# Kernel tuning notes

Measured on AMD Instinct MI355X. Metric: run time of the kernel, lower is better.

The kernel has to match this reference:

```python
import jax, jax.numpy as jnp
import numpy as np

B, S, E, H, WIN = 1, 2048, 1024, 16, 256
D = E // H  # head_out = 64


def setup_inputs() -> dict:
    key = jax.random.key(0)
    ks = jax.random.split(key, 10)
    w = lambda k: jax.random.normal(k, (E, E), jnp.float32) * 0.02
    return {
        'x': jax.random.normal(ks[0], (B, S, E), jnp.float32),
        'global_attention_mask': jax.random.randint(ks[1], (B, S), 0, 2).astype(jnp.int32),
        'W_local_query': w(ks[2]),
        'W_local_key': w(ks[3]),
        'W_local_value': w(ks[4]),
        'W_query': w(ks[5]),
        'W_key': w(ks[6]),
        'W_value': w(ks[7]),
        'W_proj': w(ks[8]),
        'b_proj': jnp.zeros((E,), jnp.float32),
    }


def reference(x, global_attention_mask, W_local_query, W_local_key, W_local_value,
              W_query, W_key, W_value, W_proj, b_proj):
    b, seq, emb = x.shape
    nH, dh, win = H, D, WIN
    chunks = seq // win
    NEG = -1e9
    scale = 1.0 / (dh ** 0.5)

    # ---- local (windowed) branch ----
    ql = x @ W_local_query            # [b,S,E]
    kl = x @ W_local_key
    vl = x @ W_local_value
    # NOTE: original does a direct .view -> plain reshape (no head transpose)
    qc = ql.reshape(b, nH, chunks, win, dh)
    kc = kl.reshape(b, nH, chunks, win, dh)
    vloc = vl.reshape(b, nH, seq, dh)
    s = jnp.einsum('bhcqd,bhckd->bhcqk', qc, kc)      # [b,H,C,W,W]
    causal_w = jnp.tril(jnp.ones((win, win), bool))
    s = jnp.where(causal_w, s, NEG) * scale           # mask then /sqrt(d), as in source
    s = s.mean(axis=2)                                # mean over chunks -> [b,H,W,W]
    s = jnp.pad(s, ((0, 0), (0, 0), (0, seq - win), (0, seq - win)))
    aw_l = jax.nn.softmax(s, axis=-1)                 # [b,H,S,S]
    local_ctx = jnp.einsum('bhqk,bhkd->bqhd', aw_l, vloc).reshape(b, seq, emb)

    # ---- global (full) branch ----
    q = (x @ W_query).reshape(b, seq, nH, dh).transpose(0, 2, 1, 3)
    k = (x @ W_key).reshape(b, seq, nH, dh).transpose(0, 2, 1, 3)
    v = (x @ W_value).reshape(b, seq, nH, dh).transpose(0, 2, 1, 3)
    sg = jnp.einsum('bhqd,bhkd->bhqk', q, k)          # [b,H,S,S]
    causal_s = jnp.tril(jnp.ones((seq, seq), bool))
    sg = jnp.where(causal_s, sg, NEG) * scale
    aw_g = jax.nn.softmax(sg, axis=-1)
    gctx = jnp.einsum('bhqk,bhkd->bqhd', aw_g, v).reshape(b, seq, emb)

    # ---- combine via global mask, then output projection ----
    ctx = jnp.where(global_attention_mask[:, :, None] == 1, gctx, local_ctx)
    return ctx @ W_proj + b_proj
```

## Files before the change

kernel.cpp:

```cpp
#include <hip/hip_runtime.h>
#include <hip/hip_bf16.h>

typedef _Float16 h8 __attribute__((ext_vector_type(8)));
typedef _Float16 h4 __attribute__((ext_vector_type(4)));
typedef _Float16 h2 __attribute__((ext_vector_type(2)));
typedef __fp16 fp16x2 __attribute__((ext_vector_type(2)));
typedef float f4 __attribute__((ext_vector_type(4)));

#define S_LEN 2048
#define EMB 1024
#define NH 16
#define DH 64

__device__ __forceinline__ void async_copy16(const void* g, void* l) {
  __builtin_amdgcn_global_load_lds(
      (const __attribute__((address_space(1))) void*)g,
      (__attribute__((address_space(3))) void*)l, 16, 0, 0);
}

__device__ __forceinline__ f4 mfma16(h8 a, h8 b, f4 c) {
  return __builtin_amdgcn_mfma_f32_16x16x32_f16(a, b, c, 0, 0, 0);
}

__device__ __forceinline__ h2 cvt_pk(float a, float b) {
  const fp16x2 r = __builtin_amdgcn_cvt_pkrtz(a, b);
  return __builtin_bit_cast(h2, r);
}

__global__ __launch_bounds__(256) void prep_kernel(
    const float* __restrict__ x, const float* w0, const float* w1, const float* w2,
    const float* w3, const float* w4, const float* w5, const float* w6,
    _Float16* __restrict__ xh, _Float16* __restrict__ Wtb) {
  const int bid = blockIdx.x;
  if (bid < 2048) {
    const int i = bid * 256 + threadIdx.x;
    const float4 v = *(const float4*)&x[(long)i * 4];
    h4 o;
    o.x = (_Float16)v.x; o.y = (_Float16)v.y; o.z = (_Float16)v.z; o.w = (_Float16)v.w;
    *(h4*)&xh[(long)i * 4] = o;
    return;
  }
  const int b2 = bid - 2048;
  const int z = b2 >> 10, rem = b2 & 1023;
  const float* W = w0;
  switch (z) {
    case 1: W = w1; break; case 2: W = w2; break; case 3: W = w3; break;
    case 4: W = w4; break; case 5: W = w5; break; case 6: W = w6; break;
    default: break;
  }
  __shared__ float t[32][33];
  const int bk = (rem & 31) * 32, bn = (rem >> 5) * 32;
  const int tx = threadIdx.x & 31, ty = threadIdx.x >> 5;
  #pragma unroll
  for (int i = 0; i < 4; ++i)
    t[ty + i * 8][tx] = W[(long)(bk + ty + i * 8) * 1024 + bn + tx];
  __syncthreads();
  _Float16* o = Wtb + (long)z * 1048576;
  #pragma unroll
  for (int i = 0; i < 4; ++i)
    o[(long)(bn + ty + i * 8) * 1024 + bk + tx] = (_Float16)t[tx][ty + i * 8];
}

__global__ __launch_bounds__(256) void shuffle_kernel(
    const _Float16* __restrict__ ql, const _Float16* __restrict__ kl,
    const _Float16* __restrict__ vl, const _Float16* __restrict__ vg,
    const int* __restrict__ gmask,
    _Float16* __restrict__ Aq, _Float16* __restrict__ Ak,
    _Float16* __restrict__ vgT, float* __restrict__ Vall, float* __restrict__ Vtail,
    int* __restrict__ qsel, int* __restrict__ qcnt) {
  const int bid = blockIdx.x;
  if (bid < 2048) {
    const _Float16* src = (bid >= 1024) ? kl : ql;
    _Float16* dst = (bid >= 1024) ? Ak : Aq;
    const int u = (bid & 1023) * 256 + threadIdx.x;
    const int dseg = u & 7, c = (u >> 3) & 7, q = (u >> 6) & 255, h = u >> 14;
    const long soff = (long)(h * 128 + c * 16 + (q >> 4)) * 1024 + (q & 15) * 64 + dseg * 8;
    *(h8*)&dst[(long)u * 8] = *(const h8*)&src[soff];
    return;
  }
  if (bid < 4096) {
    const int b2 = bid - 2048;
    __shared__ _Float16 t[32][33];
    const int bs = (b2 & 63) * 32, be = (b2 >> 6) * 32;
    const int tx = threadIdx.x & 31, ty = threadIdx.x >> 5;
    #pragma unroll
    for (int i = 0; i < 4; ++i)
      t[ty + i * 8][tx] = vg[(long)(bs + ty + i * 8) * 1024 + be + tx];
    __syncthreads();
    #pragma unroll
    for (int i = 0; i < 4; ++i)
      vgT[(long)(be + ty + i * 8) * 2048 + bs + tx] = t[tx][ty + i * 8];
    return;
  }
  if (bid < 4112) {
    const int hh = bid - 4096;
    const int d = threadIdx.x & 63, g = threadIdx.x >> 6;
    float sall = 0.f, shead = 0.f;
    for (int i = 0; i < 32; ++i) {
      const int ro = g * 32 + i;
      const _Float16* base = vl + (long)(hh * 128 + ro) * 1024 + d;
      #pragma unroll
      for (int j = 0; j < 16; ++j) {
        const float v = (float)base[j * 64];
        sall += v;
        if (ro < 16) shead += v;
      }
    }
    __shared__ float sA[4][64], sH[4][64];
    sA[g][d] = sall; sH[g][d] = shead;
    __syncthreads();
    if (g == 0) {
      const float a = sA[0][d] + sA[1][d] + sA[2][d] + sA[3][d];
      const float hsum = sH[0][d] + sH[1][d] + sH[2][d] + sH[3][d];
      Vall[hh * 64 + d] = a;
      Vtail[hh * 64 + d] = a - hsum;
    }
    return;
  }
  const int t = threadIdx.x;
  int m8[8], cnt8 = 0;
  #pragma unroll
  for (int j = 0; j < 8; ++j) {
    m8[j] = gmask[t * 8 + j];
    cnt8 += (m8[j] == 1);
  }
  __shared__ int sc[256];
  sc[t] = cnt8;
  __syncthreads();
  for (int off = 1; off < 256; off <<= 1) {
    const int v = (t >= off) ? sc[t - off] : 0;
    __syncthreads();
    sc[t] += v;
    __syncthreads();
  }
  int base = sc[t] - cnt8;
  #pragma unroll
  for (int j = 0; j < 8; ++j)
    if (m8[j] == 1) qsel[base++] = t * 8 + j;
  if (t == 255) qcnt[0] = sc[255];
}

__global__ __launch_bounds__(512, 2) void gemm256_kernel(
    const _Float16* __restrict__ A, const _Float16* __restrict__ Bt,
    _Float16* __restrict__ C) {
  const int bid = blockIdx.x;
  const int bxx = (bid >> 3) & 7;
  const int byy = (bid & 7) * 3 + (bid >> 6);
  const int bm = bxx * 256, bn = byy * 256;

  __shared__ alignas(16) _Float16 As[2][2][8192];
  __shared__ alignas(16) _Float16 Bs[2][2][8192];

  const int tid = threadIdx.x;
  const int w = tid >> 6, l = tid & 63;
  const int lo = l & 15, hi = l >> 4;
  const int wm = w >> 2, wn = w & 3;
  const int srow = tid >> 3;
  const int kseg = (tid & 7) ^ (srow & 7);

  const _Float16* Bb = Bt + (long)(byy >> 2) * 1048576 + (long)(bn & 1023) * 1024;

#define STG_A(db, half, tt) do {                                                     \
    const int t_ = (tt) < 15 ? (tt) : 15;                                            \
    const _Float16* s_ = A + (long)(bm + (half) * 128 + srow) * 1024 + t_ * 64 + kseg * 8; \
    async_copy16(s_, &As[db][half][w * 512]);                                        \
    async_copy16(s_ + 65536, &As[db][half][4096 + w * 512]);                         \
  } while (0)
#define STG_B(db, half, tt) do {                                                     \
    const int t_ = (tt) < 15 ? (tt) : 15;                                            \
    const _Float16* s_ = Bb + (long)((half) * 128 + srow) * 1024 + t_ * 64 + kseg * 8; \
    async_copy16(s_, &Bs[db][half][w * 512]);                                        \
    async_copy16(s_ + 65536, &Bs[db][half][4096 + w * 512]);                         \
  } while (0)
#define LDA(db, mg) do { _Pragma("unroll")                                           \
    for (int fr = 0; fr < 4; ++fr) {                                                 \
      const int rr = wm * 64 + fr * 16 + lo;                                         \
      _Pragma("unroll") for (int kk = 0; kk < 2; ++kk)                               \
        af[fr][kk] = *(const h8*)&As[db][mg][rr * 64 + (((kk * 4 + hi) ^ (rr & 7)) * 8)]; \
    } } while (0)
#define LDB(db, ng) do { _Pragma("unroll")                                           \
    for (int fc = 0; fc < 2; ++fc) {                                                 \
      const int rr = wn * 32 + fc * 16 + lo;                                         \
      _Pragma("unroll") for (int kk = 0; kk < 2; ++kk)                               \
        bf[ng][fc][kk] = *(const h8*)&Bs[db][ng][rr * 64 + (((kk * 4 + hi) ^ (rr & 7)) * 8)]; \
    } } while (0)
#define MFMA_PH(mg, ng) do {                                                         \
    __builtin_amdgcn_s_setprio(1);                                                   \
    _Pragma("unroll") for (int fr = 0; fr < 4; ++fr)                                 \
      _Pragma("unroll") for (int fc = 0; fc < 2; ++fc) {                             \
        acc[mg][fr][ng][fc] = mfma16(af[fr][0], bf[ng][fc][0], acc[mg][fr][ng][fc]); \
        acc[mg][fr][ng][fc] = mfma16(af[fr][1], bf[ng][fc][1], acc[mg][fr][ng][fc]); \
      }                                                                              \
    __builtin_amdgcn_s_setprio(0);                                                   \
  } while (0)
#define BARR do { asm volatile("" ::: "memory"); __builtin_amdgcn_s_barrier();       \
                  asm volatile("" ::: "memory"); } while (0)
#define VM8 asm volatile("s_waitcnt vmcnt(8)" ::: "memory")

  const f4 zero = {0.f, 0.f, 0.f, 0.f};
  f4 acc[2][4][2][2];
  #pragma unroll
  for (int a_ = 0; a_ < 2; ++a_)
    #pragma unroll
    for (int b_ = 0; b_ < 4; ++b_)
      #pragma unroll
      for (int c_ = 0; c_ < 2; ++c_)
        #pragma unroll
        for (int d_ = 0; d_ < 2; ++d_) acc[a_][b_][c_][d_] = zero;
  h8 af[4][2];
  h8 bf[2][2][2];

  STG_A(0, 0, 0); STG_B(0, 0, 0); STG_A(0, 1, 0); STG_B(0, 1, 0);
  STG_A(1, 0, 1); STG_B(1, 0, 1); STG_A(1, 1, 1);
  asm volatile("s_waitcnt vmcnt(6)" ::: "memory");
  BARR;

  for (int i = 0; i < 8; ++i) {
    const int t2 = 2 * i + 2, t3 = 2 * i + 3;
    LDA(0, 0); LDB(0, 0); STG_B(1, 1, 2 * i + 1); MFMA_PH(0, 0); VM8; BARR;
    LDB(0, 1); STG_A(0, 0, t2); MFMA_PH(0, 1); BARR;
    LDA(0, 1); STG_B(0, 0, t2); MFMA_PH(1, 0); BARR;
    STG_A(0, 1, t2); MFMA_PH(1, 1); VM8; BARR;
    LDA(1, 0); LDB(1, 0); STG_B(0, 1, t2); MFMA_PH(0, 0); VM8; BARR;
    LDB(1, 1); STG_A(1, 0, t3); MFMA_PH(0, 1); BARR;
    LDA(1, 1); STG_B(1, 0, t3); MFMA_PH(1, 0); BARR;
    STG_A(1, 1, t3); MFMA_PH(1, 1); VM8; BARR;
  }

  #pragma unroll
  for (int mg = 0; mg < 2; ++mg)
    #pragma unroll
    for (int fr = 0; fr < 4; ++fr) {
      const int row = bm + mg * 128 + wm * 64 + fr * 16 + hi * 4;
      #pragma unroll
      for (int ng = 0; ng < 2; ++ng)
        #pragma unroll
        for (int fc = 0; fc < 2; ++fc) {
          const int colg = bn + ng * 128 + wn * 32 + fc * 16 + lo;
          _Float16* cp = C + (long)(colg >> 10) * 2097152 + (long)row * 1024 + (colg & 1023);
          #pragma unroll
          for (int r = 0; r < 4; ++r)
            cp[(long)r * 1024] = (_Float16)acc[mg][fr][ng][fc][r];
        }
    }
#undef STG_A
#undef STG_B
#undef LDA
#undef LDB
#undef MFMA_PH
#undef BARR
#undef VM8
}

__global__ __launch_bounds__(256) void gemm64_kernel(
    const _Float16* __restrict__ A, const _Float16* __restrict__ Bt,
    float* __restrict__ C, const float* __restrict__ bias) {
  const int bm = blockIdx.x * 64, bn = blockIdx.y * 64;
  __shared__ alignas(16) _Float16 As[2][4096];
  __shared__ alignas(16) _Float16 Bs[2][4096];
  const int tid = threadIdx.x;
  const int w = tid >> 6, l = tid & 63;
  const int lo = l & 15, hi = l >> 4;
  const int srow = tid >> 3;
  const int ssl = (tid & 7) ^ (srow & 7);

#define STG64(b, k0) do {                                                            \
    async_copy16(&A[(long)(bm + srow) * 1024 + (k0) + ssl * 8], &As[b][(w * 8) * 64]); \
    async_copy16(&A[(long)(bm + 32 + srow) * 1024 + (k0) + ssl * 8],                 \
                 &As[b][(w * 8 + 32) * 64]);                                         \
    async_copy16(&Bt[(long)(bn + srow) * 1024 + (k0) + ssl * 8], &Bs[b][(w * 8) * 64]); \
    async_copy16(&Bt[(long)(bn + 32 + srow) * 1024 + (k0) + ssl * 8],                \
                 &Bs[b][(w * 8 + 32) * 64]);                                         \
  } while (0)

  const f4 zero = {0.f, 0.f, 0.f, 0.f};
  f4 acc[4];
  #pragma unroll
  for (int n = 0; n < 4; ++n) acc[n] = zero;

  STG64(0, 0);
  __syncthreads();
  int cur = 0;
  for (int k0 = 0; k0 < 1024; k0 += 64) {
    if (k0 + 64 < 1024) STG64(cur ^ 1, k0 + 64);
    #pragma unroll
    for (int kk = 0; kk < 2; ++kk) {
      const int ra = w * 16 + lo;
      const h8 af = *(const h8*)&As[cur][ra * 64 + (((kk * 4 + hi) ^ (ra & 7)) * 8)];
      #pragma unroll
      for (int n = 0; n < 4; ++n) {
        const int rb = n * 16 + lo;
        const h8 bff = *(const h8*)&Bs[cur][rb * 64 + (((kk * 4 + hi) ^ (rb & 7)) * 8)];
        acc[n] = mfma16(af, bff, acc[n]);
      }
    }
    __syncthreads();
    cur ^= 1;
  }
#undef STG64

  #pragma unroll
  for (int n = 0; n < 4; ++n) {
    const int col = bn + n * 16 + lo;
    const float bv = bias[col];
    const int row0 = bm + w * 16 + hi * 4;
    #pragma unroll
    for (int r = 0; r < 4; ++r)
      C[(long)(row0 + r) * 1024 + col] = acc[n][r] + bv;
  }
}

__global__ __launch_bounds__(256) void flash_kernel(
    const _Float16* __restrict__ Q, const _Float16* __restrict__ Km,
    const _Float16* __restrict__ Vt, const int* __restrict__ qsel,
    const int* __restrict__ qcnt, _Float16* __restrict__ ctx,
    _Float16* __restrict__ pO, float2* __restrict__ ml,
    const _Float16* __restrict__ Aq, const _Float16* __restrict__ Ak,
    _Float16* __restrict__ P, const float* __restrict__ Vall,
    const int* __restrict__ gmask) {
  __shared__ alignas(16) char smem[43008];
  const int bx = blockIdx.x;
  const int tid = threadIdx.x;

  if (bx >= 1088) {
    const int gid = (bx - 1088) * 256 + tid;
    const int s = 256 + (gid >> 7), e8 = (gid & 127) * 8;
    if (gmask[s] == 0) {
      h8 v;
      #pragma unroll
      for (int j = 0; j < 8; ++j)
        v[j] = (_Float16)(Vall[e8 + j] * (1.f / 2048.f));
      *(h8*)&ctx[(long)s * EMB + e8] = v;
    }
    return;
  }

  if (bx >= 1024) {
    const int b = bx - 1024;
    const int bzz = b >> 2, bxx = (b >> 1) & 1, byy = b & 1;
    const _Float16* Ab = Aq + (long)bzz * 131072;
    const _Float16* Bb = Ak + (long)bzz * 131072;
    const int bm = bxx * 128, bn = byy * 128;
    _Float16* As = (_Float16*)smem;
    _Float16* Bs = (_Float16*)(smem + 16384);
    const int w = tid >> 6, l = tid & 63;
    const int lo = l & 15, hi = l >> 4;
    const int wr = (w >> 1) * 64, wc = (w & 1) * 64;
    const int srow = l >> 3, ssp = l & 7;
    const int ssl = ssp ^ (srow & 7);

    const f4 zero = {0.f, 0.f, 0.f, 0.f};
    f4 acc[4][4];
    #pragma unroll
    for (int m = 0; m < 4; ++m)
      #pragma unroll
      for (int n = 0; n < 4; ++n) acc[m][n] = zero;

    for (int k0 = 0; k0 < 512; k0 += 64) {
      #pragma unroll
      for (int i = 0; i < 4; ++i) {
        const int chunk = w + i * 4;
        async_copy16(&Ab[(long)(bm + chunk * 8 + srow) * 512 + k0 + ssl * 8], &As[chunk * 512]);
        async_copy16(&Bb[(long)(bn + chunk * 8 + srow) * 512 + k0 + ssl * 8], &Bs[chunk * 512]);
      }
      __syncthreads();
      #pragma unroll
      for (int kk = 0; kk < 2; ++kk) {
        h8 af[4], bff[4];
        #pragma unroll
        for (int m = 0; m < 4; ++m) {
          const int r = wr + m * 16 + lo;
          af[m] = *(const h8*)&As[r * 64 + (((kk * 4 + hi) ^ (r & 7)) * 8)];
        }
        #pragma unroll
        for (int n = 0; n < 4; ++n) {
          const int r = wc + n * 16 + lo;
          bff[n] = *(const h8*)&Bs[r * 64 + (((kk * 4 + hi) ^ (r & 7)) * 8)];
        }
        #pragma unroll
        for (int m = 0; m < 4; ++m)
          #pragma unroll
          for (int n = 0; n < 4; ++n)
            acc[m][n] = mfma16(af[m], bff[n], acc[m][n]);
      }
      __syncthreads();
    }
    #pragma unroll
    for (int m = 0; m < 4; ++m) {
      const int row0 = bm + wr + m * 16 + hi * 4;
      #pragma unroll
      for (int n = 0; n < 4; ++n) {
        const int col = bn + wc + n * 16 + lo;
        #pragma unroll
        for (int r = 0; r < 4; ++r)
          P[(long)bzz * 65536 + (long)(row0 + r) * 256 + col] = (_Float16)acc[m][n][r];
      }
    }
    return;
  }

  const int h = bx & 15;
  const int v = bx >> 4;
  const int tile = 31 - (v >> 1);
  const int chunk = v & 1;
  int cnt = qcnt[0];
  cnt = cnt < 1 ? 1 : (cnt > 2048 ? 2048 : cnt);
  if (tile * 64 >= cnt) return;
  const int L = (qsel[min(tile * 64 + 63, cnt - 1)] & 2047) + 1;
  const int ntot = (L + 63) >> 6;
  const bool chunked = (ntot > 16);
  if (!chunked && chunk) return;
  const int nsplit = chunked ? ((ntot + 1) >> 1) : ntot;
  const int t0 = chunk ? nsplit : 0;
  const int t1 = chunk ? ntot : nsplit;

  const int w = tid >> 6, l = tid & 63;
  const int lo = l & 15, hi = l >> 4;
  const int row = tile * 64 + w * 16 + lo;
  const int qg = qsel[min(row, cnt - 1)] & 2047;

  _Float16* KsB = (_Float16*)smem;
  _Float16* VsB = (_Float16*)(smem + 16384);
  _Float16* ps = (_Float16*)(smem + 32768) + w * 1280;

  const int rl = tid >> 3;
  const int ssl = (tid & 7) ^ (rl & 7);

#define STAGE(b, t)                                                                   \
  do {                                                                                \
    async_copy16(&Km[(long)((t) * 64 + rl) * EMB + h * DH + ssl * 8],                 \
                 &KsB[(b) * 4096 + (w * 8) * 64]);                                    \
    async_copy16(&Km[(long)((t) * 64 + 32 + rl) * EMB + h * DH + ssl * 8],            \
                 &KsB[(b) * 4096 + (w * 8 + 32) * 64]);                               \
    async_copy16(&Vt[(long)(h * DH + rl) * S_LEN + (t) * 64 + ssl * 8],               \
                 &VsB[(b) * 4096 + (w * 8) * 64]);                                    \
    async_copy16(&Vt[(long)(h * DH + 32 + rl) * S_LEN + (t) * 64 + ssl * 8],          \
                 &VsB[(b) * 4096 + (w * 8 + 32) * 64]);                               \
  } while (0)

  h8 qf[2];
  #pragma unroll
  for (int kk = 0; kk < 2; ++kk)
    qf[kk] = *(const h8*)&Q[(long)qg * EMB + h * DH + kk * 32 + hi * 8];

  const f4 zero = {0.f, 0.f, 0.f, 0.f};
  f4 o[4];
  #pragma unroll
  for (int nd = 0; nd < 4; ++nd) o[nd] = zero;
  float mr = -1e30f, lr = 0.f;
  const float SC = 0.125f * 1.44269504f;

  STAGE(0, t0);
  __syncthreads();
  int cur = 0;

  for (int t = t0; t < t1; ++t) {
    if (t + 1 < t1) STAGE(cur ^ 1, t + 1);

    const _Float16* ks = KsB + cur * 4096;
    const _Float16* vs = VsB + cur * 4096;

    __builtin_amdgcn_s_setprio(1);
    f4 s[4];
    #pragma unroll
    for (int n = 0; n < 4; ++n) {
      s[n] = zero;
      #pragma unroll
      for (int kk = 0; kk < 2; ++kk) {
        const int r = n * 16 + lo;
        const h8 kf = *(const h8*)&ks[r * 64 + (((kk * 4 + hi) ^ (lo & 7)) * 8)];
        s[n] = mfma16(kf, qf[kk], s[n]);
      }
    }
    __builtin_amdgcn_s_setprio(0);

    float sv[16];
    float tm = -1e30f;
    #pragma unroll
    for (int n = 0; n < 4; ++n)
      #pragma unroll
      for (int r = 0; r < 4; ++r) {
        float vv = s[n][r] * SC;
        if ((t * 64 + n * 16 + hi * 4 + r) > qg) vv = -1e30f;
        sv[n * 4 + r] = vv;
        tm = fmaxf(tm, vv);
      }
    tm = fmaxf(tm, __shfl_xor(tm, 16));
    tm = fmaxf(tm, __shfl_xor(tm, 32));
    const float mn = fmaxf(mr, tm);
    const float c = exp2f(mr - mn);
    mr = mn;
    float psum = 0.f;
    #pragma unroll
    for (int i = 0; i < 16; ++i) {
      sv[i] = exp2f(sv[i] - mr);
      psum += sv[i];
    }
    psum += __shfl_xor(psum, 16);
    psum += __shfl_xor(psum, 32);
    lr = lr * c + psum;

    #pragma unroll
    for (int n = 0; n < 4; ++n) {
      const int seg = (2 * n + (hi >> 1)) ^ (lo & 7);
      const int base = lo * 80 + seg * 8 + (hi & 1) * 4;
      *(h2*)&ps[base] = cvt_pk(sv[n * 4 + 0], sv[n * 4 + 1]);
      *(h2*)&ps[base + 2] = cvt_pk(sv[n * 4 + 2], sv[n * 4 + 3]);
    }
    h8 pb[2];
    #pragma unroll
    for (int kk = 0; kk < 2; ++kk)
      pb[kk] = *(const h8*)&ps[lo * 80 + (((kk * 4 + hi) ^ (lo & 7)) * 8)];

    __builtin_amdgcn_s_setprio(1);
    #pragma unroll
    for (int nd = 0; nd < 4; ++nd) {
      #pragma unroll
      for (int r = 0; r < 4; ++r) o[nd][r] *= c;
      #pragma unroll
      for (int kk = 0; kk < 2; ++kk) {
        const int rr = nd * 16 + lo;
        const h8 vf = *(const h8*)&vs[rr * 64 + (((kk * 4 + hi) ^ (lo & 7)) * 8)];
        o[nd] = mfma16(vf, pb[kk], o[nd]);
      }
    }
    __builtin_amdgcn_s_setprio(0);

    __syncthreads();
    cur ^= 1;
  }
#undef STAGE

  if (chunked) {
    const int slot = (h * 32 + tile) * 2 + chunk;
    _Float16* po = pO + (long)slot * 4096 + (w * 16 + lo) * 64;
    #pragma unroll
    for (int nd = 0; nd < 4; ++nd) {
      const h2 a = cvt_pk(o[nd][0], o[nd][1]);
      const h2 b = cvt_pk(o[nd][2], o[nd][3]);
      const h4 v4 = {a[0], a[1], b[0], b[1]};
      *(h4*)&po[nd * 16 + hi * 4] = v4;
    }
    if (hi == 0) ml[slot * 64 + w * 16 + lo] = make_float2(mr, lr);
  } else if (row < cnt) {
    const float inv = 1.f / lr;
    #pragma unroll
    for (int nd = 0; nd < 4; ++nd) {
      const h2 a = cvt_pk(o[nd][0] * inv, o[nd][1] * inv);
      const h2 b = cvt_pk(o[nd][2] * inv, o[nd][3] * inv);
      const h4 v4 = {a[0], a[1], b[0], b[1]};
      *(h4*)&ctx[(long)qg * EMB + h * DH + nd * 16 + hi * 4] = v4;
    }
  }
}

__global__ __launch_bounds__(256) void localfin_kernel(
    const _Float16* __restrict__ P, const _Float16* __restrict__ vl,
    const float* __restrict__ Vtail,
    const _Float16* __restrict__ pO, const float2* __restrict__ ml,
    const int* __restrict__ gmask, const int* __restrict__ qsel,
    const int* __restrict__ qcnt, _Float16* __restrict__ ctx) {
  const int bid = blockIdx.x;
  const int tid = threadIdx.x;
  if (bid < 1024) {
    const int q = bid & 255, hg = bid >> 8;
    if (gmask[q] == 1) return;
    const int sub = tid >> 6, l = tid & 63;
    const int hh = hg * 4 + sub;
    __shared__ float wgt[4][256];
    const _Float16* Pr = P + ((long)hh * 256 + q) * 256;
    float sv[4];
    bool valid[4];
    float M = -1e30f;
    #pragma unroll
    for (int i = 0; i < 4; ++i) {
      const int k = l + i * 64;
      valid[i] = (k <= q);
      sv[i] = valid[i] ? (float)Pr[k] * 0.015625f : -1e30f;
      M = fmaxf(M, sv[i]);
    }
    M = fmaxf(M, __shfl_xor(M, 1));
    M = fmaxf(M, __shfl_xor(M, 2));
    M = fmaxf(M, __shfl_xor(M, 4));
    M = fmaxf(M, __shfl_xor(M, 8));
    M = fmaxf(M, __shfl_xor(M, 16));
    M = fmaxf(M, __shfl_xor(M, 32));
    M = fmaxf(M, 0.f);
    float ps = 0.f;
    #pragma unroll
    for (int i = 0; i < 4; ++i) {
      const float e = valid[i] ? __expf(sv[i] - M) : 0.f;
      wgt[sub][l + i * 64] = e;
      ps += e;
    }
    ps += __shfl_xor(ps, 1);
    ps += __shfl_xor(ps, 2);
    ps += __shfl_xor(ps, 4);
    ps += __shfl_xor(ps, 8);
    ps += __shfl_xor(ps, 16);
    ps += __shfl_xor(ps, 32);
    const float em = __expf(-M);
    const float denom = ps + 1792.f * em;
    const int d = l;
    float acc = em * Vtail[hh * 64 + d];
    const _Float16* vb = vl + (long)hh * 128 * 1024 + d;
    for (int k = 0; k <= q; ++k)
      acc += wgt[sub][k] * (float)vb[(long)(k >> 4) * 1024 + (k & 15) * 64];
    ctx[(long)q * EMB + hh * DH + d] = (_Float16)(acc / denom);
    return;
  }
  const int b2 = bid - 1024;
  const int h = b2 & 15, tile = b2 >> 4;
  int cnt = qcnt[0];
  cnt = cnt < 1 ? 1 : (cnt > 2048 ? 2048 : cnt);
  if (tile * 64 >= cnt) return;
  const int L = (qsel[min(tile * 64 + 63, cnt - 1)] & 2047) + 1;
  if (((L + 63) >> 6) <= 16) return;
  const int q = tid >> 2, ds = (tid & 3) * 16;
  const int row = tile * 64 + q;
  if (row >= cnt) return;
  const int sg = qsel[row] & 2047;
  const int slot0 = (h * 32 + tile) * 2, slot1 = slot0 + 1;
  const float2 ml0 = ml[slot0 * 64 + q];
  const float2 ml1 = ml[slot1 * 64 + q];
  const float M = fmaxf(ml0.x, ml1.x);
  const float w0 = exp2f(ml0.x - M), w1 = exp2f(ml1.x - M);
  const float inv = 1.f / (w0 * ml0.y + w1 * ml1.y);
  const h8 a0 = *(const h8*)&pO[(long)slot0 * 4096 + q * 64 + ds];
  const h8 a1 = *(const h8*)&pO[(long)slot0 * 4096 + q * 64 + ds + 8];
  const h8 b0 = *(const h8*)&pO[(long)slot1 * 4096 + q * 64 + ds];
  const h8 b1 = *(const h8*)&pO[(long)slot1 * 4096 + q * 64 + ds + 8];
  h8 r0, r1;
  #pragma unroll
  for (int j = 0; j < 8; ++j) {
    r0[j] = (_Float16)((w0 * (float)a0[j] + w1 * (float)b0[j]) * inv);
    r1[j] = (_Float16)((w0 * (float)a1[j] + w1 * (float)b1[j]) * inv);
  }
  *(h8*)&ctx[(long)sg * EMB + h * DH + ds] = r0;
  *(h8*)&ctx[(long)sg * EMB + h * DH + ds + 8] = r1;
}

extern "C" void kernel_launch(void* const* d_in, const int* in_sizes, int n_in,
                              void* d_out, int out_size, void* d_ws, size_t ws_size,
                              hipStream_t stream) {
  const float* x = (const float*)d_in[0];
  const int* gmask = (const int*)d_in[1];
  const float* Wlq = (const float*)d_in[2];
  const float* Wlk = (const float*)d_in[3];
  const float* Wlv = (const float*)d_in[4];
  const float* Wq = (const float*)d_in[5];
  const float* Wk = (const float*)d_in[6];
  const float* Wv = (const float*)d_in[7];
  const float* Wp = (const float*)d_in[8];
  const float* bp = (const float*)d_in[9];
  float* out = (float*)d_out;

  char* ws = (char*)d_ws;
  _Float16* xh = (_Float16*)(ws);
  _Float16* Wtb = (_Float16*)(ws + (4u << 20));
  _Float16* proj = (_Float16*)(ws + (18u << 20));
  _Float16* ql = proj;
  _Float16* kl = (_Float16*)(ws + (22u << 20));
  _Float16* vl = (_Float16*)(ws + (26u << 20));
  _Float16* qg = (_Float16*)(ws + (30u << 20));
  _Float16* kg = (_Float16*)(ws + (34u << 20));
  _Float16* vg = (_Float16*)(ws + (38u << 20));
  _Float16* Aq = (_Float16*)(ws + (4u << 20));
  _Float16* Ak = (_Float16*)(ws + (8u << 20));
  _Float16* P = (_Float16*)(ws + (12u << 20));
  float* Vall = (float*)(ws + (14u << 20));
  float* Vtail = (float*)(ws + (14u << 20) + 4096);
  float2* ml = (float2*)(ws + (14u << 20) + 16384);
  int* qsel = (int*)(ws + (14u << 20) + 614400);
  int* qcnt = (int*)(ws + (14u << 20) + 622592);
  _Float16* Wpt = (_Float16*)(ws + (16u << 20));
  _Float16* vgT = (_Float16*)(ws);
  _Float16* ctx = (_Float16*)(ws + (18u << 20));
  _Float16* pO = (_Float16*)(ws + (38u << 20));

  prep_kernel<<<9216, 256, 0, stream>>>(x, Wlq, Wlk, Wlv, Wq, Wk, Wv, Wp, xh, Wtb);
  gemm256_kernel<<<192, 512, 0, stream>>>(xh, Wtb, proj);
  shuffle_kernel<<<4113, 256, 0, stream>>>(ql, kl, vl, vg, gmask, Aq, Ak, vgT,
                                           Vall, Vtail, qsel, qcnt);
  flash_kernel<<<1984, 256, 0, stream>>>(qg, kg, vgT, qsel, qcnt, ctx, pO, ml,
                                         Aq, Ak, P, Vall, gmask);
  localfin_kernel<<<1536, 256, 0, stream>>>(P, vl, Vtail, pO, ml, gmask,
                                            qsel, qcnt, ctx);
  gemm64_kernel<<<dim3(32, 16), 256, 0, stream>>>(ctx, Wpt, out, bp);
}
```

Baseline: 123.8 us.

## Eliminate shuffle kernel by fusing layout transforms into GEMM epilogue

New measurement: 116.2 us, median of 2. -6.1%, faster.

```diff
diff --git a/kernel.cpp b/kernel.cpp
--- a/kernel.cpp
+++ b/kernel.cpp
@@ -30,7 +30,8 @@
 __global__ __launch_bounds__(256) void prep_kernel(
     const float* __restrict__ x, const float* w0, const float* w1, const float* w2,
     const float* w3, const float* w4, const float* w5, const float* w6,
-    _Float16* __restrict__ xh, _Float16* __restrict__ Wtb) {
+    _Float16* __restrict__ xh, _Float16* __restrict__ Wtb,
+    const int* __restrict__ gmask, int* __restrict__ qsel, int* __restrict__ qcnt) {
   const int bid = blockIdx.x;
   if (bid < 2048) {
     const int i = bid * 256 + threadIdx.x;
@@ -40,81 +41,26 @@
     *(h4*)&xh[(long)i * 4] = o;
     return;
   }
-  const int b2 = bid - 2048;
-  const int z = b2 >> 10, rem = b2 & 1023;
-  const float* W = w0;
-  switch (z) {
-    case 1: W = w1; break; case 2: W = w2; break; case 3: W = w3; break;
-    case 4: W = w4; break; case 5: W = w5; break; case 6: W = w6; break;
-    default: break;
-  }
-  __shared__ float t[32][33];
-  const int bk = (rem & 31) * 32, bn = (rem >> 5) * 32;
-  const int tx = threadIdx.x & 31, ty = threadIdx.x >> 5;
-  #pragma unroll
-  for (int i = 0; i < 4; ++i)
-    t[ty + i * 8][tx] = W[(long)(bk + ty + i * 8) * 1024 + bn + tx];
-  __syncthreads();
-  _Float16* o = Wtb + (long)z * 1048576;
-  #pragma unroll
-  for (int i = 0; i < 4; ++i)
-    o[(long)(bn + ty + i * 8) * 1024 + bk + tx] = (_Float16)t[tx][ty + i * 8];
-}
-
-__global__ __launch_bounds__(256) void shuffle_kernel(
-    const _Float16* __restrict__ ql, const _Float16* __restrict__ kl,
-    const _Float16* __restrict__ vl, const _Float16* __restrict__ vg,
-    const int* __restrict__ gmask,
-    _Float16* __restrict__ Aq, _Float16* __restrict__ Ak,
-    _Float16* __restrict__ vgT, float* __restrict__ Vall, float* __restrict__ Vtail,
-    int* __restrict__ qsel, int* __restrict__ qcnt) {
-  const int bid = blockIdx.x;
-  if (bid < 2048) {
-    const _Float16* src = (bid >= 1024) ? kl : ql;
-    _Float16* dst = (bid >= 1024) ? Ak : Aq;
-    const int u = (bid & 1023) * 256 + threadIdx.x;
-    const int dseg = u & 7, c = (u >> 3) & 7, q = (u >> 6) & 255, h = u >> 14;
-    const long soff = (long)(h * 128 + c * 16 + (q >> 4)) * 1024 + (q & 15) * 64 + dseg * 8;
-    *(h8*)&dst[(long)u * 8] = *(const h8*)&src[soff];
-    return;
-  }
-  if (bid < 4096) {
+  if (bid < 9216) {
     const int b2 = bid - 2048;
-    __shared__ _Float16 t[32][33];
-    const int bs = (b2 & 63) * 32, be = (b2 >> 6) * 32;
+    const int z = b2 >> 10, rem = b2 & 1023;
+    const float* W = w0;
+    switch (z) {
+      case 1: W = w1; break; case 2: W = w2; break; case 3: W = w3; break;
+      case 4: W = w4; break; case 5: W = w5; break; case 6: W = w6; break;
+      default: break;
+    }
+    __shared__ float t[32][33];
+    const int bk = (rem & 31) * 32, bn = (rem >> 5) * 32;
     const int tx = threadIdx.x & 31, ty = threadIdx.x >> 5;
     #pragma unroll
     for (int i = 0; i < 4; ++i)
-      t[ty + i * 8][tx] = vg[(long)(bs + ty + i * 8) * 1024 + be + tx];
+      t[ty + i * 8][tx] = W[(long)(bk + ty + i * 8) * 1024 + bn + tx];
     __syncthreads();
+    _Float16* o = Wtb + (long)z * 1048576;
     #pragma unroll
     for (int i = 0; i < 4; ++i)
-      vgT[(long)(be + ty + i * 8) * 2048 + bs + tx] = t[tx][ty + i * 8];
-    return;
-  }
-  if (bid < 4112) {
-    const int hh = bid - 4096;
-    const int d = threadIdx.x & 63, g = threadIdx.x >> 6;
-    float sall = 0.f, shead = 0.f;
-    for (int i = 0; i < 32; ++i) {
-      const int ro = g * 32 + i;
-      const _Float16* base = vl + (long)(hh * 128 + ro) * 1024 + d;
-      #pragma unroll
-      for (int j = 0; j < 16; ++j) {
-        const float v = (float)base[j * 64];
-        sall += v;
-        if (ro < 16) shead += v;
-      }
-    }
-    __shared__ float sA[4][64], sH[4][64];
-    sA[g][d] = sall; sH[g][d] = shead;
-    __syncthreads();
-    if (g == 0) {
-      const float a = sA[0][d] + sA[1][d] + sA[2][d] + sA[3][d];
-      const float hsum = sH[0][d] + sH[1][d] + sH[2][d] + sH[3][d];
-      Vall[hh * 64 + d] = a;
-      Vtail[hh * 64 + d] = a - hsum;
-    }
+      o[(long)(bn + ty + i * 8) * 1024 + bk + tx] = (_Float16)t[tx][ty + i * 8];
     return;
   }
   const int t = threadIdx.x;
@@ -142,7 +88,8 @@
 
 __global__ __launch_bounds__(512, 2) void gemm256_kernel(
     const _Float16* __restrict__ A, const _Float16* __restrict__ Bt,
-    _Float16* __restrict__ C) {
+    _Float16* __restrict__ Aq, _Float16* __restrict__ Ak,
+    _Float16* __restrict__ proj234, _Float16* __restrict__ vgT) {
   const int bid = blockIdx.x;
   const int bxx = (bid >> 3) & 7;
   const int byy = (bid & 7) * 3 + (bid >> 6);
@@ -227,20 +174,38 @@
     STG_A(1, 1, t3); MFMA_PH(1, 1); VM8; BARR;
   }
 
+  const int slabv = byy >> 2;
   #pragma unroll
   for (int mg = 0; mg < 2; ++mg)
     #pragma unroll
     for (int fr = 0; fr < 4; ++fr) {
-      const int row = bm + mg * 128 + wm * 64 + fr * 16 + hi * 4;
+      const int row0 = bm + mg * 128 + wm * 64 + fr * 16 + hi * 4;
       #pragma unroll
       for (int ng = 0; ng < 2; ++ng)
         #pragma unroll
         for (int fc = 0; fc < 2; ++fc) {
           const int colg = bn + ng * 128 + wn * 32 + fc * 16 + lo;
-          _Float16* cp = C + (long)(colg >> 10) * 2097152 + (long)row * 1024 + (colg & 1023);
-          #pragma unroll
-          for (int r = 0; r < 4; ++r)
-            cp[(long)r * 1024] = (_Float16)acc[mg][fr][ng][fc][r];
+          const int e = colg & 1023;
+          if (slabv <= 1) {
+            _Float16* dst = (slabv == 0) ? Aq : Ak;
+            #pragma unroll
+            for (int r = 0; r < 4; ++r) {
+              const int s = row0 + r;
+              const long off = (long)(((s >> 7) * 256 + (s & 15) * 16 + (e >> 6))) * 512
+                               + ((s >> 4) & 7) * 64 + (e & 63);
+              dst[off] = (_Float16)acc[mg][fr][ng][fc][r];
+            }
+          } else if (slabv == 5) {
+            const h2 a = cvt_pk(acc[mg][fr][ng][fc][0], acc[mg][fr][ng][fc][1]);
+            const h2 b = cvt_pk(acc[mg][fr][ng][fc][2], acc[mg][fr][ng][fc][3]);
+            const h4 v4 = {a[0], a[1], b[0], b[1]};
+            *(h4*)&vgT[(long)e * 2048 + row0] = v4;
+          } else {
+            _Float16* cp = proj234 + (long)(slabv - 2) * 2097152 + (long)row0 * 1024 + e;
+            #pragma unroll
+            for (int r = 0; r < 4; ++r)
+              cp[(long)r * 1024] = (_Float16)acc[mg][fr][ng][fc][r];
+          }
         }
     }
 #undef STG_A
@@ -316,21 +281,35 @@
     const int* __restrict__ qcnt, _Float16* __restrict__ ctx,
     _Float16* __restrict__ pO, float2* __restrict__ ml,
     const _Float16* __restrict__ Aq, const _Float16* __restrict__ Ak,
-    _Float16* __restrict__ P, const float* __restrict__ Vall,
-    const int* __restrict__ gmask) {
+    _Float16* __restrict__ P, const _Float16* __restrict__ vl,
+    float* __restrict__ Vall, float* __restrict__ Vtail) {
   __shared__ alignas(16) char smem[43008];
   const int bx = blockIdx.x;
   const int tid = threadIdx.x;
 
   if (bx >= 1088) {
-    const int gid = (bx - 1088) * 256 + tid;
-    const int s = 256 + (gid >> 7), e8 = (gid & 127) * 8;
-    if (gmask[s] == 0) {
-      h8 v;
-      #pragma unroll
-      for (int j = 0; j < 8; ++j)
-        v[j] = (_Float16)(Vall[e8 + j] * (1.f / 2048.f));
-      *(h8*)&ctx[(long)s * EMB + e8] = v;
+    const int hh = bx - 1088;
+    const int d = tid & 63, g = tid >> 6;
+    float sall = 0.f, shead = 0.f;
+    for (int i = 0; i < 32; ++i) {
+      const int ro = g * 32 + i;
+      const _Float16* base = vl + (long)(hh * 128 + ro) * 1024 + d;
+      #pragma unroll
+      for (int j = 0; j < 16; ++j) {
+        const float v = (float)base[j * 64];
+        sall += v;
+        if (ro < 16) shead += v;
+      }
+    }
+    float* sA = (float*)smem;
+    float* sH = (float*)(smem + 1024);
+    sA[g * 64 + d] = sall; sH[g * 64 + d] = shead;
+    __syncthreads();
+    if (g == 0) {
+      const float a = sA[d] + sA[64 + d] + sA[128 + d] + sA[192 + d];
+      const float hsum = sH[d] + sH[64 + d] + sH[128 + d] + sH[192 + d];
+      Vall[hh * 64 + d] = a;
+      Vtail[hh * 64 + d] = a - hsum;
     }
     return;
   }
@@ -556,7 +535,7 @@
 
 __global__ __launch_bounds__(256) void localfin_kernel(
     const _Float16* __restrict__ P, const _Float16* __restrict__ vl,
-    const float* __restrict__ Vtail,
+    const float* __restrict__ Vall, const float* __restrict__ Vtail,
     const _Float16* __restrict__ pO, const float2* __restrict__ ml,
     const int* __restrict__ gmask, const int* __restrict__ qsel,
     const int* __restrict__ qcnt, _Float16* __restrict__ ctx) {
@@ -609,35 +588,47 @@
     ctx[(long)q * EMB + hh * DH + d] = (_Float16)(acc / denom);
     return;
   }
-  const int b2 = bid - 1024;
-  const int h = b2 & 15, tile = b2 >> 4;
-  int cnt = qcnt[0];
-  cnt = cnt < 1 ? 1 : (cnt > 2048 ? 2048 : cnt);
-  if (tile * 64 >= cnt) return;
-  const int L = (qsel[min(tile * 64 + 63, cnt - 1)] & 2047) + 1;
-  if (((L + 63) >> 6) <= 16) return;
-  const int q = tid >> 2, ds = (tid & 3) * 16;
-  const int row = tile * 64 + q;
-  if (row >= cnt) return;
-  const int sg = qsel[row] & 2047;
-  const int slot0 = (h * 32 + tile) * 2, slot1 = slot0 + 1;
-  const float2 ml0 = ml[slot0 * 64 + q];
-  const float2 ml1 = ml[slot1 * 64 + q];
-  const float M = fmaxf(ml0.x, ml1.x);
-  const float w0 = exp2f(ml0.x - M), w1 = exp2f(ml1.x - M);
-  const float inv = 1.f / (w0 * ml0.y + w1 * ml1.y);
-  const h8 a0 = *(const h8*)&pO[(long)slot0 * 4096 + q * 64 + ds];
-  const h8 a1 = *(const h8*)&pO[(long)slot0 * 4096 + q * 64 + ds + 8];
-  const h8 b0 = *(const h8*)&pO[(long)slot1 * 4096 + q * 64 + ds];
-  const h8 b1 = *(const h8*)&pO[(long)slot1 * 4096 + q * 64 + ds + 8];
-  h8 r0, r1;
-  #pragma unroll
-  for (int j = 0; j < 8; ++j) {
-    r0[j] = (_Float16)((w0 * (float)a0[j] + w1 * (float)b0[j]) * inv);
-    r1[j] = (_Float16)((w0 * (float)a1[j] + w1 * (float)b1[j]) * inv);
-  }
-  *(h8*)&ctx[(long)sg * EMB + h * DH + ds] = r0;
-  *(h8*)&ctx[(long)sg * EMB + h * DH + ds + 8] = r1;
+  if (bid < 1536) {
+    const int b2 = bid - 1024;
+    const int h = b2 & 15, tile = b2 >> 4;
+    int cnt = qcnt[0];
+    cnt = cnt < 1 ? 1 : (cnt > 2048 ? 2048 : cnt);
+    if (tile * 64 >= cnt) return;
+    const int L = (qsel[min(tile * 64 + 63, cnt - 1)] & 2047) + 1;
+    if (((L + 63) >> 6) <= 16) return;
+    const int q = tid >> 2, ds = (tid & 3) * 16;
+    const int row = tile * 64 + q;
+    if (row >= cnt) return;
+    const int sg = qsel[row] & 2047;
+    const int slot0 = (h * 32 + tile) * 2, slot1 = slot0 + 1;
+    const float2 ml0 = ml[slot0 * 64 + q];
+    const float2 ml1 = ml[slot1 * 64 + q];
+    const float M = fmaxf(ml0.x, ml1.x);
+    const float w0 = exp2f(ml0.x - M), w1 = exp2f(ml1.x - M);
+    const float inv = 1.f / (w0 * ml0.y + w1 * ml1.y);
+    const h8 a0 = *(const h8*)&pO[(long)slot0 * 4096 + q * 64 + ds];
+    const h8 a1 = *(const h8*)&pO[(long)slot0 * 4096 + q * 64 + ds + 8];
+    const h8 b0 = *(const h8*)&pO[(long)slot1 * 4096 + q * 64 + ds];
+    const h8 b1 = *(const h8*)&pO[(long)slot1 * 4096 + q * 64 + ds + 8];
+    h8 r0, r1;
+    #pragma unroll
+    for (int j = 0; j < 8; ++j) {
+      r0[j] = (_Float16)((w0 * (float)a0[j] + w1 * (float)b0[j]) * inv);
+      r1[j] = (_Float16)((w0 * (float)a1[j] + w1 * (float)b1[j]) * inv);
+    }
+    *(h8*)&ctx[(long)sg * EMB + h * DH + ds] = r0;
+    *(h8*)&ctx[(long)sg * EMB + h * DH + ds + 8] = r1;
+    return;
+  }
+  const int gid = (bid - 1536) * 256 + tid;
+  const int s = 256 + (gid >> 7), e8 = (gid & 127) * 8;
+  if (gmask[s] == 0) {
+    h8 v;
+    #pragma unroll
+    for (int j = 0; j < 8; ++j)
+      v[j] = (_Float16)(Vall[e8 + j] * (1.f / 2048.f));
+    *(h8*)&ctx[(long)s * EMB + e8] = v;
+  }
 }
 
 extern "C" void kernel_launch(void* const* d_in, const int* in_sizes, int n_in,
@@ -658,33 +649,29 @@
   char* ws = (char*)d_ws;
   _Float16* xh = (_Float16*)(ws);
   _Float16* Wtb = (_Float16*)(ws + (4u << 20));
-  _Float16* proj = (_Float16*)(ws + (18u << 20));
-  _Float16* ql = proj;
-  _Float16* kl = (_Float16*)(ws + (22u << 20));
-  _Float16* vl = (_Float16*)(ws + (26u << 20));
-  _Float16* qg = (_Float16*)(ws + (30u << 20));
-  _Float16* kg = (_Float16*)(ws + (34u << 20));
-  _Float16* vg = (_Float16*)(ws + (38u << 20));
-  _Float16* Aq = (_Float16*)(ws + (4u << 20));
-  _Float16* Ak = (_Float16*)(ws + (8u << 20));
+  _Float16* pO = (_Float16*)(ws);
+  _Float16* ctx = (_Float16*)(ws + (8u << 20));
   _Float16* P = (_Float16*)(ws + (12u << 20));
   float* Vall = (float*)(ws + (14u << 20));
   float* Vtail = (float*)(ws + (14u << 20) + 4096);
   float2* ml = (float2*)(ws + (14u << 20) + 16384);
-  int* qsel = (int*)(ws + (14u << 20) + 614400);
-  int* qcnt = (int*)(ws + (14u << 20) + 622592);
   _Float16* Wpt = (_Float16*)(ws + (16u << 20));
-  _Float16* vgT = (_Float16*)(ws);
-  _Float16* ctx = (_Float16*)(ws + (18u << 20));
-  _Float16* pO = (_Float16*)(ws + (38u << 20));
-
-  prep_kernel<<<9216, 256, 0, stream>>>(x, Wlq, Wlk, Wlv, Wq, Wk, Wv, Wp, xh, Wtb);
-  gemm256_kernel<<<192, 512, 0, stream>>>(xh, Wtb, proj);
-  shuffle_kernel<<<4113, 256, 0, stream>>>(ql, kl, vl, vg, gmask, Aq, Ak, vgT,
-                                           Vall, Vtail, qsel, qcnt);
-  flash_kernel<<<1984, 256, 0, stream>>>(qg, kg, vgT, qsel, qcnt, ctx, pO, ml,
-                                         Aq, Ak, P, Vall, gmask);
-  localfin_kernel<<<1536, 256, 0, stream>>>(P, vl, Vtail, pO, ml, gmask,
+  _Float16* Aq = (_Float16*)(ws + (18u << 20));
+  _Float16* Ak = (_Float16*)(ws + (22u << 20));
+  _Float16* proj234 = (_Float16*)(ws + (26u << 20));
+  _Float16* vl = proj234;
+  _Float16* qg = (_Float16*)(ws + (30u << 20));
+  _Float16* kg = (_Float16*)(ws + (34u << 20));
+  _Float16* vgT = (_Float16*)(ws + (38u << 20));
+  int* qsel = (int*)(ws + (42u << 20));
+  int* qcnt = (int*)(ws + (42u << 20) + 8192);
+
+  prep_kernel<<<9217, 256, 0, stream>>>(x, Wlq, Wlk, Wlv, Wq, Wk, Wv, Wp, xh, Wtb,
+                                        gmask, qsel, qcnt);
+  gemm256_kernel<<<192, 512, 0, stream>>>(xh, Wtb, Aq, Ak, proj234, vgT);
+  flash_kernel<<<1104, 256, 0, stream>>>(qg, kg, vgT, qsel, qcnt, ctx, pO, ml,
+                                         Aq, Ak, P, vl, Vall, Vtail);
+  localfin_kernel<<<2432, 256, 0, stream>>>(P, vl, Vall, Vtail, pO, ml, gmask,
                                             qsel, qcnt, ctx);
   gemm64_kernel<<<dim3(32, 16), 256, 0, stream>>>(ctx, Wpt, out, bp);
 }
```
